# Optimization experiments

Measured on AMD Instinct MI355X. Metric: run time of the kernel, lower is better.

The kernel has to match this reference:

```python
import jax, jax.numpy as jnp
import numpy as np

IN_DIM, HID, HEADS, OUT_DIM = 768, 128, 4, 256
SEM = HID * HEADS  # 512
N_USER, N_LLM, E = 50000, 5000, 400000


def gat_conv(x_src, x_dst, src, dst, W_src, W_dst, att_src, att_dst, bias, n_dst):
    """PyG GATConv (bipartite, concat=True), eval mode (no dropout)."""
    H, C = att_src.shape
    hs = (x_src @ W_src).reshape(-1, H, C)  # [Ns,H,C]
    hd = (x_dst @ W_dst).reshape(-1, H, C)  # [Nd,H,C]
    a_s = (hs * att_src).sum(-1)            # [Ns,H]
    a_d = (hd * att_dst).sum(-1)            # [Nd,H]
    e = jax.nn.leaky_relu(a_s[src] + a_d[dst], 0.2)  # [E,H]
    m = jax.ops.segment_max(e, dst, num_segments=n_dst)
    m = jnp.where(jnp.isfinite(m), m, 0.0)
    ex = jnp.exp(e - m[dst])
    denom = jax.ops.segment_sum(ex, dst, num_segments=n_dst)
    alpha = ex / (denom[dst] + 1e-16)        # [E,H]
    msg = hs[src] * alpha[:, :, None]        # [E,H,C]
    out = jax.ops.segment_sum(msg, dst, num_segments=n_dst)  # [Nd,H,C]
    return out.reshape(n_dst, H * C) + bias


def setup_inputs() -> dict:
    key = jax.random.key(0)
    ks = jax.random.split(key, 20)
    s = lambda k, shape, sc: jax.random.normal(k, shape, jnp.float32) * sc
    d = {
        'x_user': jax.random.normal(ks[0], (N_USER, IN_DIM), jnp.float32),
        'x_llm': jax.random.normal(ks[1], (N_LLM, IN_DIM), jnp.float32),
        'src0': jax.random.randint(ks[2], (E,), 0, N_LLM, jnp.int32),
        'dst0': jax.random.randint(ks[3], (E,), 0, N_USER, jnp.int32),
        'src1': jax.random.randint(ks[4], (E,), 0, N_USER, jnp.int32),
        'dst1': jax.random.randint(ks[5], (E,), 0, N_USER, jnp.int32),
    }
    sc_in = 1.0 / np.sqrt(IN_DIM)
    for i in range(2):
        d[f'Wsrc{i}'] = s(ks[6 + 5 * i], (IN_DIM, HEADS * HID), sc_in)
        d[f'Wdst{i}'] = s(ks[7 + 5 * i], (IN_DIM, HEADS * HID), sc_in)
        d[f'asrc{i}'] = s(ks[8 + 5 * i], (HEADS, HID), 1.0 / np.sqrt(HID))
        d[f'adst{i}'] = s(ks[9 + 5 * i], (HEADS, HID), 1.0 / np.sqrt(HID))
        d[f'bias{i}'] = jnp.zeros((HEADS * HID,), jnp.float32)
    d['sem_W1'] = s(ks[16], (SEM, 128), 1.0 / np.sqrt(SEM))
    d['sem_b1'] = jnp.zeros((128,), jnp.float32)
    d['sem_W2'] = s(ks[17], (128, 1), 1.0 / np.sqrt(128))
    d['out_W'] = s(ks[18], (SEM, OUT_DIM), 1.0 / np.sqrt(SEM))
    d['out_b'] = jnp.zeros((OUT_DIM,), jnp.float32)
    return d


def reference(x_user, x_llm, src0, dst0, src1, dst1,
              Wsrc0, Wdst0, asrc0, adst0, bias0,
              Wsrc1, Wdst1, asrc1, adst1, bias1,
              sem_W1, sem_b1, sem_W2, out_W, out_b):
    # metapath 0: llm -> user ; metapath 1: user -> user
    z0 = jax.nn.elu(gat_conv(x_llm, x_user, src0, dst0,
                             Wsrc0, Wdst0, asrc0, adst0, bias0, N_USER))
    z1 = jax.nn.elu(gat_conv(x_user, x_user, src1, dst1,
                             Wsrc1, Wdst1, asrc1, adst1, bias1, N_USER))
    z = jnp.stack([z0, z1], axis=1)  # [N, P=2, SEM]
    w = jnp.tanh(z @ sem_W1 + sem_b1) @ sem_W2  # [N,P,1]
    beta = jax.nn.softmax(w, axis=1)
    z_final = (beta * z).sum(axis=1)  # [N, SEM]
    return z_final @ out_W + out_b    # [N, OUT_DIM]
```

## Files before the change

kernel.cpp:

```cpp
#include <hip/hip_runtime.h>
#include <hip/hip_bf16.h>
#include <math.h>

constexpr int IN_DIM  = 768;
constexpr int HID     = 128;
constexpr int OUT_DIM = 256;
constexpr int SEM     = 512;
constexpr int N_USER  = 50000;
constexpr int N_LLM   = 5000;
constexpr int NE      = 400000;

constexpr int MP_USER = 50048;
constexpr int MP_LLM  = 5120;
constexpr int MP_2U   = 100096;
constexpr int GY_USER = MP_USER / 128;
constexpr int GY_LLM  = MP_LLM / 128;

typedef unsigned int uint;
typedef unsigned short ushort;
typedef __attribute__((ext_vector_type(8))) short bf16x8;
typedef __attribute__((ext_vector_type(4))) float f32x4;

constexpr int cdiv(int a, int b) { return (a + b - 1) / b; }

__device__ __forceinline__ ushort f2b(float f) {
  uint u = __float_as_uint(f);
  u += 0x7FFFu + ((u >> 16) & 1u);
  return (ushort)(u >> 16);
}
__device__ __forceinline__ float b2f(uint bits16) {
  return __uint_as_float(bits16 << 16);
}

__device__ __forceinline__ float fexp2(float x) { return __builtin_amdgcn_exp2f(x); }
#define LOG2E 1.4426950408889634f

#define GLOAD_LDS16(g, l) __builtin_amdgcn_global_load_lds( \
    (const __attribute__((address_space(1))) void*)(g), \
    (__attribute__((address_space(3))) void*)(l), 16, 0, 0)


constexpr int GX_HS  = 5;
constexpr int NWG_HS = GX_HS * (GY_USER + GY_LLM);
constexpr int NB_SC  = cdiv(2 * NE, 256);
__global__ __launch_bounds__(256) void gemm_hs_sc(
    const ushort* __restrict__ A_u, const ushort* __restrict__ A_l,
    const ushort* __restrict__ Bt_u, const ushort* __restrict__ Bt_l,
    ushort* __restrict__ hs_u, ushort* __restrict__ hs_l,
    float* __restrict__ logU, float* __restrict__ logL,
    const int* __restrict__ src0, const int* __restrict__ dst0,
    const int* __restrict__ src1, const int* __restrict__ dst1,
    const int* __restrict__ rp, const int* __restrict__ rank,
    ushort* __restrict__ scsr)
{
  const int t = threadIdx.x;
  if (blockIdx.x >= NWG_HS) {
    int e = (blockIdx.x - NWG_HS) * 256 + t;
    if (e < 2 * NE) {
      bool p1 = (e >= NE);
      int ee = p1 ? e - NE : e;
      int s = p1 ? src1[ee] : src0[ee];
      int d = p1 ? (dst1[ee] + N_USER) : dst0[ee];
      scsr[rp[d] + rank[e]] = (ushort)s;
    }
    return;
  }

  __shared__ ushort As[128][64];
  __shared__ ushort Bs[128][64];
  const int wid = t >> 6, lane = t & 63;
  const int K = IN_DIM;

  const int nwg  = NWG_HS;
  const int orig = blockIdx.x;
  const int q = nwg >> 3, r = nwg & 7;
  const int xcd = orig & 7, idx = orig >> 3;
  const int swz = (xcd < r ? xcd * (q + 1) : r * (q + 1) + (xcd - r) * q) + idx;
  const int bxi = swz % GX_HS, byi0 = swz / GX_HS;

  const bool llm = (byi0 >= GY_USER);
  const int byi = llm ? byi0 - GY_USER : byi0;
  const ushort* A    = llm ? A_l : A_u;
  const ushort* Bt   = llm ? Bt_l : Bt_u;
  ushort* hs         = llm ? hs_l : hs_u;
  float* logit       = llm ? logL : logU;

  const int bm = byi * 128, bn = bxi * 128;
  const int lr = lane & 15, kg = lane >> 4;
  const int sw8 = lr & 7;
  const int mbase = (wid >> 1) * 64, nbase = (wid & 1) * 64;
  const int grow = lane >> 3;
  const int gcol = (((lane & 7) ^ grow)) * 8;

  f32x4 acc[4][4] = {};

  for (int k0 = 0; k0 < K; k0 += 64) {
#pragma unroll
    for (int c = 0; c < 4; ++c) {
      int ch = wid * 4 + c;
      GLOAD_LDS16(A  + (size_t)(bm + ch * 8 + grow) * K + k0 + gcol, &As[ch * 8][0]);
      GLOAD_LDS16(Bt + (size_t)(bn + ch * 8 + grow) * K + k0 + gcol, &Bs[ch * 8][0]);
    }
    asm volatile("s_waitcnt vmcnt(0)" ::: "memory");
    __syncthreads();
#pragma unroll
    for (int kb = 0; kb < 2; ++kb) {
      const int csw = ((kb * 4 + kg) ^ sw8) * 8;
      bf16x8 av[4], bv[4];
#pragma unroll
      for (int m = 0; m < 4; ++m)
        av[m] = *(const bf16x8*)&As[mbase + m * 16 + lr][csw];
#pragma unroll
      for (int n = 0; n < 4; ++n)
        bv[n] = *(const bf16x8*)&Bs[nbase + n * 16 + lr][csw];
#pragma unroll
      for (int m = 0; m < 4; ++m)
#pragma unroll
        for (int n = 0; n < 4; ++n)
          acc[m][n] = __builtin_amdgcn_mfma_f32_16x16x32_bf16(av[m], bv[n], acc[m][n], 0, 0, 0);
    }
    __syncthreads();
  }

  if (bxi == GX_HS - 1) {
    if (nbase == 0) {
#pragma unroll
      for (int m = 0; m < 4; ++m)
#pragma unroll
        for (int j = 0; j < 4; ++j) {
          int row = bm + mbase + m * 16 + kg * 4 + j;
          logit[(size_t)row * 16 + lr] = acc[m][0][j];
        }
    }
    return;
  }

#pragma unroll
  for (int m = 0; m < 4; ++m)
#pragma unroll
    for (int j = 0; j < 4; ++j) {
      int row = bm + mbase + m * 16 + kg * 4 + j;
#pragma unroll
      for (int n = 0; n < 4; ++n) {
        int col = bn + nbase + n * 16 + lr;
        hs[(size_t)row * SEM + col] = f2b(acc[m][n][j]);
      }
    }
}

__global__ __launch_bounds__(256) void gemm_beta(
    const ushort* __restrict__ Z, const ushort* __restrict__ WtS,
    const float* __restrict__ b1, const float* __restrict__ W2,
    float2* __restrict__ beta)
{
  __shared__ ushort As[128][64];
  __shared__ ushort Bs[128][64];
  __shared__ float wsum[128][2];
  const int t = threadIdx.x;
  const int wid = t >> 6, lane = t & 63;
  const int K = SEM;

  const int nwg  = gridDim.x;
  const int orig = blockIdx.x;
  const int q = nwg >> 3, r = nwg & 7;
  const int xcd = orig & 7, idx = orig >> 3;
  const int swz = (xcd < r ? xcd * (q + 1) : r * (q + 1) + (xcd - r) * q) + idx;

  const int bm = swz * 128;
  const int lr = lane & 15, kg = lane >> 4;
  const int sw8 = lr & 7;
  const int mbase = (wid >> 1) * 64, nbase = (wid & 1) * 64;
  const int grow = lane >> 3;
  const int gcol = (((lane & 7) ^ grow)) * 8;

  f32x4 acc[4][4] = {};

  for (int k0 = 0; k0 < K; k0 += 64) {
#pragma unroll
    for (int c = 0; c < 4; ++c) {
      int ch = wid * 4 + c;
      GLOAD_LDS16(Z   + (size_t)(bm + ch * 8 + grow) * K + k0 + gcol, &As[ch * 8][0]);
      GLOAD_LDS16(WtS + (size_t)(ch * 8 + grow) * K + k0 + gcol, &Bs[ch * 8][0]);
    }
    asm volatile("s_waitcnt vmcnt(0)" ::: "memory");
    __syncthreads();
#pragma unroll
    for (int kb = 0; kb < 2; ++kb) {
      const int csw = ((kb * 4 + kg) ^ sw8) * 8;
      bf16x8 av[4], bv[4];
#pragma unroll
      for (int m = 0; m < 4; ++m)
        av[m] = *(const bf16x8*)&As[mbase + m * 16 + lr][csw];
#pragma unroll
      for (int n = 0; n < 4; ++n)
        bv[n] = *(const bf16x8*)&Bs[nbase + n * 16 + lr][csw];
#pragma unroll
      for (int m = 0; m < 4; ++m)
#pragma unroll
        for (int n = 0; n < 4; ++n)
          acc[m][n] = __builtin_amdgcn_mfma_f32_16x16x32_bf16(av[m], bv[n], acc[m][n], 0, 0, 0);
    }
    __syncthreads();
  }

  float part[4][4];
#pragma unroll
  for (int m = 0; m < 4; ++m)
#pragma unroll
    for (int j = 0; j < 4; ++j) {
      float s = 0.f;
#pragma unroll
      for (int n = 0; n < 4; ++n) {
        int col = nbase + n * 16 + lr;
        float tv = acc[m][n][j] + b1[col];
        tv = fminf(fmaxf(tv, -20.f), 20.f);
        float e = fexp2(2.f * LOG2E * tv);
        s += ((e - 1.f) / (e + 1.f)) * W2[col];
      }
      part[m][j] = s;
    }
#pragma unroll
  for (int off = 1; off < 16; off <<= 1)
#pragma unroll
    for (int m = 0; m < 4; ++m)
#pragma unroll
      for (int j = 0; j < 4; ++j)
        part[m][j] += __shfl_xor(part[m][j], off);
  if (lr == 0) {
#pragma unroll
    for (int m = 0; m < 4; ++m)
#pragma unroll
      for (int j = 0; j < 4; ++j)
        wsum[mbase + m * 16 + kg * 4 + j][wid & 1] = part[m][j];
  }
  __syncthreads();
  if (t < 64) {
    float w0 = wsum[2 * t][0] + wsum[2 * t][1];
    float w1 = wsum[2 * t + 1][0] + wsum[2 * t + 1][1];
    float mx = fmaxf(w0, w1);
    float e0 = fexp2((w0 - mx) * LOG2E), e1 = fexp2((w1 - mx) * LOG2E);
    float s = e0 + e1;
    beta[swz * 64 + t] = make_float2(e0 / s, e1 / s);
  }
}

__global__ __launch_bounds__(256) void gemm_out(
    const ushort* __restrict__ Z, const ushort* __restrict__ WtO,
    float* __restrict__ out, const float* __restrict__ out_b,
    const float2* __restrict__ beta)
{
  __shared__ ushort As[128][64];
  __shared__ ushort Bs[256][64];
  const int t = threadIdx.x;
  const int wid = t >> 6, lane = t & 63;
  const int K = SEM;

  const int nwg  = gridDim.x;
  const int orig = blockIdx.x;
  const int q = nwg >> 3, r = nwg & 7;
  const int xcd = orig & 7, idx = orig >> 3;
  const int swz = (xcd < r ? xcd * (q + 1) : r * (q + 1) + (xcd - r) * q) + idx;

  const int bm = swz * 128;
  const int lr = lane & 15, kg = lane >> 4;
  const int sw8 = lr & 7;
  const int mbase = (wid >> 1) * 64, nbase = (wid & 1) * 128;
  const int grow = lane >> 3;
  const int gcol = (((lane & 7) ^ grow)) * 8;
  const int wcol = (((lane & 7) ^ grow)) * 8;

  f32x4 acc[4][8] = {};

  for (int k0 = 0; k0 < K; k0 += 64) {
#pragma unroll
    for (int c = 0; c < 8; ++c) {
      int ch = wid * 8 + c;
      GLOAD_LDS16(WtO + (size_t)(ch * 8 + grow) * K + k0 + gcol, &Bs[ch * 8][0]);
    }
#pragma unroll
    for (int c = 0; c < 4; ++c) {
      int ch = wid * 4 + c;
      int rl = ch * 8 + grow;
      int row = bm + rl;
      const ushort* z0p = Z + (size_t)(2 * row) * SEM + k0 + (lane & 7) * 8;
      const ushort* z1p = z0p + SEM;
      float2 bb = beta[row];
      uint4 a0 = *(const uint4*)z0p;
      uint4 a1 = *(const uint4*)z1p;
      uint rpk[4];
#pragma unroll
      for (int qq = 0; qq < 4; ++qq) {
        uint x0 = ((const uint*)&a0)[qq], x1 = ((const uint*)&a1)[qq];
        float lo = bb.x * b2f(x0 & 0xffffu) + bb.y * b2f(x1 & 0xffffu);
        float hi = bb.x * b2f(x0 >> 16)     + bb.y * b2f(x1 >> 16);
        rpk[qq] = (uint)f2b(lo) | ((uint)f2b(hi) << 16);
      }
      *(uint4*)&As[rl][wcol] = make_uint4(rpk[0], rpk[1], rpk[2], rpk[3]);
    }
    asm volatile("s_waitcnt vmcnt(0)" ::: "memory");
    __syncthreads();
#pragma unroll
    for (int kb = 0; kb < 2; ++kb) {
      const int csw = ((kb * 4 + kg) ^ sw8) * 8;
      bf16x8 av[4], bv[8];
#pragma unroll
      for (int m = 0; m < 4; ++m)
        av[m] = *(const bf16x8*)&As[mbase + m * 16 + lr][csw];
#pragma unroll
      for (int n = 0; n < 8; ++n)
        bv[n] = *(const bf16x8*)&Bs[nbase + n * 16 + lr][csw];
#pragma unroll
      for (int m = 0; m < 4; ++m)
#pragma unroll
        for (int n = 0; n < 8; ++n)
          acc[m][n] = __builtin_amdgcn_mfma_f32_16x16x32_bf16(av[m], bv[n], acc[m][n], 0, 0, 0);
    }
    __syncthreads();
  }

#pragma unroll
  for (int m = 0; m < 4; ++m)
#pragma unroll
    for (int j = 0; j < 4; ++j) {
      int row = bm + mbase + m * 16 + kg * 4 + j;
      if (row >= N_USER) continue;
#pragma unroll
      for (int n = 0; n < 8; ++n) {
        int col = nbase + n * 16 + lr;
        out[(size_t)row * OUT_DIM + col] = acc[m][n][j] + out_b[col];
      }
    }
}

constexpr int NB_FOLD  = cdiv(IN_DIM * 16, 256);
constexpr int NB_CASTU = N_USER * IN_DIM / 8 / 256;
constexpr int NB_CASTL = N_LLM * IN_DIM / 8 / 256;
constexpr int NB_TTW   = (IN_DIM / 64) * (SEM / 64);
constexpr int NB_TTS   = (SEM / 64) * (HID / 64);
constexpr int NB_TTO   = (SEM / 64) * (OUT_DIM / 64);
constexpr int NB_E1    = cdiv(2 * NE, 256);
constexpr int PB0 = NB_FOLD;
constexpr int PB1 = PB0 + NB_CASTU;
constexpr int PB2 = PB1 + NB_CASTL;
constexpr int PB3 = PB2 + NB_TTW;
constexpr int PB4 = PB3 + NB_TTW;
constexpr int PB5 = PB4 + NB_TTS;
constexpr int PB6 = PB5 + NB_TTO;
constexpr int PB7 = PB6 + NB_E1;
constexpr int PREP_GRID = 2048;

__device__ __forceinline__ void tt_body(const float* __restrict__ W,
                                        ushort* __restrict__ Bt,
                                        int K, int Nw, int tile,
                                        float (*lds)[65], int t)
{
  const int tiles_n = Nw >> 6;
  const int tk = tile / tiles_n, tn = tile - tk * tiles_n;
  const int k0 = tk << 6, n0 = tn << 6;
#pragma unroll
  for (int i = 0; i < 16; ++i) {
    int idx = t + i * 256;
    int rr = idx >> 6, cc = idx & 63;
    lds[rr][cc] = W[(size_t)(k0 + rr) * Nw + n0 + cc];
  }
  __syncthreads();
#pragma unroll
  for (int i = 0; i < 4; ++i) {
    int idx = t + i * 256;
    int cc = idx >> 4;
    int rq = (idx & 15) * 4;
    uint lo = (uint)f2b(lds[rq][cc])     | ((uint)f2b(lds[rq + 1][cc]) << 16);
    uint hi = (uint)f2b(lds[rq + 2][cc]) | ((uint)f2b(lds[rq + 3][cc]) << 16);
    *(uint2*)(Bt + (size_t)(n0 + cc) * K + k0 + rq) = make_uint2(lo, hi);
  }
  __syncthreads();
}

__device__ __forceinline__ void cast_body(const float* __restrict__ x,
                                          ushort* __restrict__ xb, int i)
{
  const float4 a = *(const float4*)(x + (size_t)i * 8);
  const float4 c = *(const float4*)(x + (size_t)i * 8 + 4);
  uint4 o;
  o.x = (uint)f2b(a.x) | ((uint)f2b(a.y) << 16);
  o.y = (uint)f2b(a.z) | ((uint)f2b(a.w) << 16);
  o.z = (uint)f2b(c.x) | ((uint)f2b(c.y) << 16);
  o.w = (uint)f2b(c.z) | ((uint)f2b(c.w) << 16);
  *(uint4*)(xb + (size_t)i * 8) = o;
}

__global__ __launch_bounds__(256) void prep_kernel(
    const float* __restrict__ x_user, const float* __restrict__ x_llm,
    ushort* __restrict__ xb_u, ushort* __restrict__ xb_l,
    const float* __restrict__ Wdst0, const float* __restrict__ adst0,
    const float* __restrict__ Wdst1, const float* __restrict__ adst1,
    const float* __restrict__ Wsrc1, const float* __restrict__ asrc1,
    const float* __restrict__ Wsrc0, const float* __restrict__ asrc0,
    ushort* __restrict__ Wt1x, ushort* __restrict__ Wt0x,
    const float* __restrict__ sem_W1, ushort* __restrict__ WtS,
    const float* __restrict__ out_W, ushort* __restrict__ WtO,
    const int* __restrict__ dst0, const int* __restrict__ dst1,
    int* __restrict__ deg, int* __restrict__ rank)
{
  __shared__ float lds[64][65];
  const int t = threadIdx.x;
  for (int b = blockIdx.x; b < PB7; b += PREP_GRID) {
    if (b < PB0) {
      int idxg = b * 256 + t;
      if (idxg < IN_DIM * 16) {
        int k = idxg >> 4, hh = idxg & 15;
        const float* W;
        const float* att;
        if (hh < 4)       { W = Wdst0; att = adst0; }
        else if (hh < 8)  { W = Wdst1; att = adst1; }
        else if (hh < 12) { W = Wsrc1; att = asrc1; }
        else              { W = Wsrc0; att = asrc0; }
        int h = hh & 3;
        float s = 0.f;
#pragma unroll 4
        for (int c = 0; c < HID; ++c)
          s += W[(size_t)k * SEM + h * HID + c] * att[h * HID + c];
        if (hh < 12) Wt1x[(size_t)(512 + hh) * IN_DIM + k] = f2b(s);
        else         Wt0x[(size_t)(512 + h) * IN_DIM + k] = f2b(s);
      }
    } else if (b < PB1) {
      cast_body(x_user, xb_u, (b - PB0) * 256 + t);
    } else if (b < PB2) {
      cast_body(x_llm, xb_l, (b - PB1) * 256 + t);
    } else if (b < PB3) {
      tt_body(Wsrc0, Wt0x, IN_DIM, SEM, b - PB2, lds, t);
    } else if (b < PB4) {
      tt_body(Wsrc1, Wt1x, IN_DIM, SEM, b - PB3, lds, t);
    } else if (b < PB5) {
      tt_body(sem_W1, WtS, SEM, HID, b - PB4, lds, t);
    } else if (b < PB6) {
      tt_body(out_W, WtO, SEM, OUT_DIM, b - PB5, lds, t);
    } else {
      int e = (b - PB6) * 256 + t;
      if (e < 2 * NE) {
        int d = (e < NE) ? dst0[e] : (dst1[e - NE] + N_USER);
        rank[e] = atomicAdd(&deg[d], 1);
      }
    }
  }
}

__global__ __launch_bounds__(256) void scan1(const int* __restrict__ deg,
                                             int* __restrict__ bsum, int n)
{
  __shared__ int sm[256];
  int b = blockIdx.x, t = threadIdx.x;
  int base = b * 1024 + t * 4;
  int s = 0;
#pragma unroll
  for (int i = 0; i < 4; ++i) if (base + i < n) s += deg[base + i];
  sm[t] = s;
  __syncthreads();
  for (int off = 128; off > 0; off >>= 1) {
    if (t < off) sm[t] += sm[t + off];
    __syncthreads();
  }
  if (t == 0) bsum[b] = sm[0];
}

__global__ __launch_bounds__(128) void scan2(const int* __restrict__ bsum,
                                             int* __restrict__ boff, int nb,
                                             int* __restrict__ rp_tail, int tailval)
{
  __shared__ int sm[128];
  int t = threadIdx.x;
  int v = (t < nb) ? bsum[t] : 0;
  sm[t] = v;
  __syncthreads();
  for (int off = 1; off < 128; off <<= 1) {
    int x = (t >= off) ? sm[t - off] : 0;
    __syncthreads();
    sm[t] += x;
    __syncthreads();
  }
  if (t < nb) boff[t] = sm[t] - v;
  if (t == 0) *rp_tail = tailval;
}

__global__ __launch_bounds__(256) void scan3(const int* __restrict__ deg,
                                             const int* __restrict__ boff,
                                             int* __restrict__ rp, int n)
{
  __shared__ int sm[256];
  int b = blockIdx.x, t = threadIdx.x;
  int base = b * 1024 + t * 4;
  int v[4];
#pragma unroll
  for (int i = 0; i < 4; ++i) v[i] = (base + i < n) ? deg[base + i] : 0;
  int tsum = v[0] + v[1] + v[2] + v[3];
  sm[t] = tsum;
  __syncthreads();
  for (int off = 1; off < 256; off <<= 1) {
    int x = (t >= off) ? sm[t - off] : 0;
    __syncthreads();
    sm[t] += x;
    __syncthreads();
  }
  int run = sm[t] - tsum + boff[b];
#pragma unroll
  for (int i = 0; i < 4; ++i) {
    if (base + i < n) rp[base + i] = run;
    run += v[i];
  }
}

__global__ __launch_bounds__(64) void agg_kernel(
    const ushort* __restrict__ hs0, const ushort* __restrict__ hs1,
    const ushort* __restrict__ srcs,
    const float* __restrict__ logitL, const float* __restrict__ logitU,
    const int* __restrict__ rp,
    const float* __restrict__ bias0, const float* __restrict__ bias1,
    ushort* __restrict__ Zout)
{
  __shared__ ushort s_src[64];
  __shared__ float  s_ev[64][4];
  int node = blockIdx.x, lane = threadIdx.x;
  bool p1 = (node >= N_USER);
  const ushort* hs   = p1 ? hs1 : hs0;
  const float*  bias = p1 ? bias1 : bias0;
  int nd = p1 ? node - N_USER : node;
  float4 ad4 = *(const float4*)(logitU + (size_t)nd * 16 + (p1 ? 4 : 0));
  ad4.x *= LOG2E; ad4.y *= LOG2E; ad4.z *= LOG2E; ad4.w *= LOG2E;
  const float* asbase = p1 ? (logitU + 8) : logitL;
  int h  = lane >> 4;
  int cb = lane * 8;
  float acc[8] = {};
  float dsum = 0.f;
  int jb = rp[node], je = rp[node + 1];
  for (int j0 = jb; j0 < je; j0 += 64) {
    int n = min(64, je - j0);
    __syncthreads();
    if (lane < n) {
      int s = srcs[j0 + lane];
      s_src[lane] = (ushort)s;
      float4 as4 = *(const float4*)(asbase + (size_t)s * 16);
      float v0 = as4.x * LOG2E + ad4.x, v1 = as4.y * LOG2E + ad4.y;
      float v2 = as4.z * LOG2E + ad4.z, v3 = as4.w * LOG2E + ad4.w;
      v0 = (v0 > 0.f) ? v0 : 0.2f * v0;
      v1 = (v1 > 0.f) ? v1 : 0.2f * v1;
      v2 = (v2 > 0.f) ? v2 : 0.2f * v2;
      v3 = (v3 > 0.f) ? v3 : 0.2f * v3;
      s_ev[lane][0] = fexp2(v0);
      s_ev[lane][1] = fexp2(v1);
      s_ev[lane][2] = fexp2(v2);
      s_ev[lane][3] = fexp2(v3);
    }
    __syncthreads();
#pragma unroll 4
    for (int j = 0; j < n; ++j) {
      int s = __builtin_amdgcn_readfirstlane((int)s_src[j]);
      float e = s_ev[j][h];
      const uint4 pv = *(const uint4*)(hs + ((size_t)s << 9) + cb);
      acc[0] += b2f(pv.x & 0xffffu) * e;  acc[1] += b2f(pv.x >> 16) * e;
      acc[2] += b2f(pv.y & 0xffffu) * e;  acc[3] += b2f(pv.y >> 16) * e;
      acc[4] += b2f(pv.z & 0xffffu) * e;  acc[5] += b2f(pv.z >> 16) * e;
      acc[6] += b2f(pv.w & 0xffffu) * e;  acc[7] += b2f(pv.w >> 16) * e;
      dsum += e;
    }
  }
  float inv = 1.f / (dsum + 1e-16f);
  float4 b4a = *(const float4*)(bias + cb);
  float4 b4b = *(const float4*)(bias + cb + 4);
  float bb[8] = { b4a.x, b4a.y, b4a.z, b4a.w, b4b.x, b4b.y, b4b.z, b4b.w };
  uint4 o;
  uint* op = (uint*)&o;
#pragma unroll
  for (int i = 0; i < 4; ++i) {
    float z0 = acc[2 * i]     * inv + bb[2 * i];
    float z1 = acc[2 * i + 1] * inv + bb[2 * i + 1];
    z0 = (z0 > 0.f) ? z0 : fexp2(z0 * LOG2E) - 1.f;
    z1 = (z1 > 0.f) ? z1 : fexp2(z1 * LOG2E) - 1.f;
    op[i] = (uint)f2b(z0) | ((uint)f2b(z1) << 16);
  }
  int zrow = 2 * nd + (p1 ? 1 : 0);
  *(uint4*)(Zout + (size_t)zrow * SEM + cb) = o;
}

extern "C" void kernel_launch(void* const* d_in, const int* in_sizes, int n_in,
                              void* d_out, int out_size, void* d_ws, size_t ws_size,
                              hipStream_t stream)
{
  const float* x_user = (const float*)d_in[0];
  const float* x_llm  = (const float*)d_in[1];
  const int* src0 = (const int*)d_in[2];
  const int* dst0 = (const int*)d_in[3];
  const int* src1 = (const int*)d_in[4];
  const int* dst1 = (const int*)d_in[5];
  const float* Wsrc0 = (const float*)d_in[6];
  const float* Wdst0 = (const float*)d_in[7];
  const float* asrc0 = (const float*)d_in[8];
  const float* adst0 = (const float*)d_in[9];
  const float* bias0 = (const float*)d_in[10];
  const float* Wsrc1 = (const float*)d_in[11];
  const float* Wdst1 = (const float*)d_in[12];
  const float* asrc1 = (const float*)d_in[13];
  const float* adst1 = (const float*)d_in[14];
  const float* bias1 = (const float*)d_in[15];
  const float* sem_W1 = (const float*)d_in[16];
  const float* sem_b1 = (const float*)d_in[17];
  const float* sem_W2 = (const float*)d_in[18];
  const float* out_W  = (const float*)d_in[19];
  const float* out_b  = (const float*)d_in[20];

  char* ws = (char*)d_ws;
  size_t off = 0;
  auto alloc = [&](size_t bytes) -> size_t {
    size_t o = off;
    off += (bytes + 255) & ~(size_t)255;
    return o;
  };

  size_t xbu_off  = alloc((size_t)MP_USER * IN_DIM * 2);
  size_t xbl_off  = alloc((size_t)MP_LLM  * IN_DIM * 2);
  size_t wt0_off  = alloc((size_t)640 * IN_DIM * 2);
  size_t wt1_off  = alloc((size_t)640 * IN_DIM * 2);
  size_t wts_off  = alloc((size_t)HID * SEM * 2);
  size_t wto_off  = alloc((size_t)OUT_DIM * SEM * 2);
  size_t hs0_off  = alloc((size_t)MP_LLM  * SEM * 2);
  size_t hs1_off  = alloc((size_t)MP_USER * SEM * 2);
  size_t Z_off    = alloc((size_t)MP_2U   * SEM * 2);
  size_t sc_off   = alloc((size_t)2 * NE * 2);
  size_t rank_off = alloc((size_t)2 * NE * 4);
  size_t lgu_off  = alloc((size_t)MP_USER * 16 * 4);
  size_t lgl_off  = alloc((size_t)MP_LLM  * 16 * 4);
  size_t beta_off = alloc((size_t)MP_USER * 8);
  size_t deg_off  = alloc((size_t)2 * N_USER * 4);
  size_t zero_end = off;
  size_t rp_off   = alloc((size_t)(2 * N_USER + 1) * 4);
  size_t bs_off   = alloc((size_t)128 * 4);
  size_t bo_off   = alloc((size_t)128 * 4);

  ushort* xb_u  = (ushort*)(ws + xbu_off);
  ushort* xb_l  = (ushort*)(ws + xbl_off);
  ushort* Wt0x  = (ushort*)(ws + wt0_off);
  ushort* Wt1x  = (ushort*)(ws + wt1_off);
  ushort* WtS   = (ushort*)(ws + wts_off);
  ushort* WtO   = (ushort*)(ws + wto_off);
  ushort* hs0b  = (ushort*)(ws + hs0_off);
  ushort* hs1b  = (ushort*)(ws + hs1_off);
  ushort* Zsw   = (ushort*)(ws + Z_off);
  ushort* scsr  = (ushort*)(ws + sc_off);
  int*    rank  = (int*)(ws + rank_off);
  float*  logU  = (float*)(ws + lgu_off);
  float*  logL  = (float*)(ws + lgl_off);
  float2* beta  = (float2*)(ws + beta_off);
  int*    deg   = (int*)(ws + deg_off);
  int*    rp    = (int*)(ws + rp_off);
  int*    bsum  = (int*)(ws + bs_off);
  int*    boff  = (int*)(ws + bo_off);

  hipMemsetAsync(ws + deg_off, 0, zero_end - deg_off, stream);
  hipMemsetAsync(Wt0x + (size_t)512 * IN_DIM, 0, (size_t)128 * IN_DIM * 2, stream);
  hipMemsetAsync(Wt1x + (size_t)512 * IN_DIM, 0, (size_t)128 * IN_DIM * 2, stream);

  prep_kernel<<<PREP_GRID, 256, 0, stream>>>(
      x_user, x_llm, xb_u, xb_l,
      Wdst0, adst0, Wdst1, adst1, Wsrc1, asrc1, Wsrc0, asrc0,
      Wt1x, Wt0x, sem_W1, WtS, out_W, WtO,
      dst0, dst1, deg, rank);

  const int NTOT = 2 * N_USER;
  const int NB = cdiv(NTOT, 1024);
  scan1<<<NB, 256, 0, stream>>>(deg, bsum, NTOT);
  scan2<<<1, 128, 0, stream>>>(bsum, boff, NB, rp + NTOT, 2 * NE);
  scan3<<<NB, 256, 0, stream>>>(deg, boff, rp, NTOT);

  gemm_hs_sc<<<NWG_HS + NB_SC, 256, 0, stream>>>(
      xb_u, xb_l, Wt1x, Wt0x, hs1b, hs0b, logU, logL,
      src0, dst0, src1, dst1, rp, rank, scsr);

  agg_kernel<<<NTOT, 64, 0, stream>>>(hs0b, hs1b, scsr, logL, logU, rp,
                                      bias0, bias1, Zsw);

  gemm_beta<<<MP_2U / 128, 256, 0, stream>>>(Zsw, WtS, sem_b1, sem_W2, beta);

  gemm_out<<<GY_USER, 256, 0, stream>>>(Zsw, WtO, (float*)d_out, out_b, beta);
}
```

Baseline: 372.9 us.

## Fuse semantic-attention beta GEMM and output GEMM into one kernel

Merges gemm_beta and gemm_out into a single kernel: each workgroup computes beta for its 64 nodes (128 Z rows), keeps it in LDS, then immediately does the beta-weighted combine and the output projection for those same 64 nodes. This removes one kernel launch, the global beta buffer round trip, and lets the Z tile be re-read while likely still in cache. In exchange the output GEMM tile shrinks from 128 to 64 rows per workgroup with twice the workgroups, so WtO is loaded twice as often and per-workgroup MFMA density drops; LDS use grows.

```diff
diff --git a/kernel.cpp b/kernel.cpp
--- a/kernel.cpp
+++ b/kernel.cpp
@@ -148,14 +148,16 @@
     }
 }
 
-__global__ __launch_bounds__(256) void gemm_beta(
+__global__ __launch_bounds__(256) void gemm_bo(
     const ushort* __restrict__ Z, const ushort* __restrict__ WtS,
     const float* __restrict__ b1, const float* __restrict__ W2,
-    float2* __restrict__ beta)
+    const ushort* __restrict__ WtO, float* __restrict__ out,
+    const float* __restrict__ out_b)
 {
   __shared__ ushort As[128][64];
-  __shared__ ushort Bs[128][64];
+  __shared__ ushort Bs[256][64];
   __shared__ float wsum[128][2];
+  __shared__ float2 betaL[64];
   const int t = threadIdx.x;
   const int wid = t >> 6, lane = t & 63;
   const int K = SEM;
@@ -166,170 +168,149 @@
   const int xcd = orig & 7, idx = orig >> 3;
   const int swz = (xcd < r ? xcd * (q + 1) : r * (q + 1) + (xcd - r) * q) + idx;
 
-  const int bm = swz * 128;
   const int lr = lane & 15, kg = lane >> 4;
   const int sw8 = lr & 7;
-  const int mbase = (wid >> 1) * 64, nbase = (wid & 1) * 64;
   const int grow = lane >> 3;
   const int gcol = (((lane & 7) ^ grow)) * 8;
 
-  f32x4 acc[4][4] = {};
-
-  for (int k0 = 0; k0 < K; k0 += 64) {
-#pragma unroll
-    for (int c = 0; c < 4; ++c) {
-      int ch = wid * 4 + c;
-      GLOAD_LDS16(Z   + (size_t)(bm + ch * 8 + grow) * K + k0 + gcol, &As[ch * 8][0]);
-      GLOAD_LDS16(WtS + (size_t)(ch * 8 + grow) * K + k0 + gcol, &Bs[ch * 8][0]);
-    }
-    asm volatile("s_waitcnt vmcnt(0)" ::: "memory");
-    __syncthreads();
-#pragma unroll
-    for (int kb = 0; kb < 2; ++kb) {
-      const int csw = ((kb * 4 + kg) ^ sw8) * 8;
-      bf16x8 av[4], bv[4];
+  {
+    const int bm = swz * 128;
+    const int mbase = (wid >> 1) * 64, nbase = (wid & 1) * 64;
+    f32x4 acc[4][4] = {};
+    for (int k0 = 0; k0 < K; k0 += 64) {
+#pragma unroll
+      for (int c = 0; c < 4; ++c) {
+        int ch = wid * 4 + c;
+        GLOAD_LDS16(Z   + (size_t)(bm + ch * 8 + grow) * K + k0 + gcol, &As[ch * 8][0]);
+        GLOAD_LDS16(WtS + (size_t)(ch * 8 + grow) * K + k0 + gcol, &Bs[ch * 8][0]);
+      }
+      asm volatile("s_waitcnt vmcnt(0)" ::: "memory");
+      __syncthreads();
+#pragma unroll
+      for (int kb = 0; kb < 2; ++kb) {
+        const int csw = ((kb * 4 + kg) ^ sw8) * 8;
+        bf16x8 av[4], bv[4];
+#pragma unroll
+        for (int m = 0; m < 4; ++m)
+          av[m] = *(const bf16x8*)&As[mbase + m * 16 + lr][csw];
+#pragma unroll
+        for (int n = 0; n < 4; ++n)
+          bv[n] = *(const bf16x8*)&Bs[nbase + n * 16 + lr][csw];
+#pragma unroll
+        for (int m = 0; m < 4; ++m)
+#pragma unroll
+          for (int n = 0; n < 4; ++n)
+            acc[m][n] = __builtin_amdgcn_mfma_f32_16x16x32_bf16(av[m], bv[n], acc[m][n], 0, 0, 0);
+      }
+      __syncthreads();
+    }
+
+    float part[4][4];
+#pragma unroll
+    for (int m = 0; m < 4; ++m)
+#pragma unroll
+      for (int j = 0; j < 4; ++j) {
+        float s = 0.f;
+#pragma unroll
+        for (int n = 0; n < 4; ++n) {
+          int col = nbase + n * 16 + lr;
+          float tv = acc[m][n][j] + b1[col];
+          tv = fminf(fmaxf(tv, -20.f), 20.f);
+          float e = fexp2(2.f * LOG2E * tv);
+          s += ((e - 1.f) / (e + 1.f)) * W2[col];
+        }
+        part[m][j] = s;
+      }
+#pragma unroll
+    for (int off = 1; off < 16; off <<= 1)
 #pragma unroll
       for (int m = 0; m < 4; ++m)
-        av[m] = *(const bf16x8*)&As[mbase + m * 16 + lr][csw];
-#pragma unroll
-      for (int n = 0; n < 4; ++n)
-        bv[n] = *(const bf16x8*)&Bs[nbase + n * 16 + lr][csw];
+#pragma unroll
+        for (int j = 0; j < 4; ++j)
+          part[m][j] += __shfl_xor(part[m][j], off);
+    if (lr == 0) {
 #pragma unroll
       for (int m = 0; m < 4; ++m)
 #pragma unroll
-        for (int n = 0; n < 4; ++n)
-          acc[m][n] = __builtin_amdgcn_mfma_f32_16x16x32_bf16(av[m], bv[n], acc[m][n], 0, 0, 0);
-    }
-    __syncthreads();
-  }
-
-  float part[4][4];
-#pragma unroll
-  for (int m = 0; m < 4; ++m)
-#pragma unroll
-    for (int j = 0; j < 4; ++j) {
-      float s = 0.f;
-#pragma unroll
-      for (int n = 0; n < 4; ++n) {
-        int col = nbase + n * 16 + lr;
-        float tv = acc[m][n][j] + b1[col];
-        tv = fminf(fmaxf(tv, -20.f), 20.f);
-        float e = fexp2(2.f * LOG2E * tv);
-        s += ((e - 1.f) / (e + 1.f)) * W2[col];
-      }
-      part[m][j] = s;
-    }
-#pragma unroll
-  for (int off = 1; off < 16; off <<= 1)
-#pragma unroll
-    for (int m = 0; m < 4; ++m)
-#pragma unroll
-      for (int j = 0; j < 4; ++j)
-        part[m][j] += __shfl_xor(part[m][j], off);
-  if (lr == 0) {
-#pragma unroll
-    for (int m = 0; m < 4; ++m)
-#pragma unroll
-      for (int j = 0; j < 4; ++j)
-        wsum[mbase + m * 16 + kg * 4 + j][wid & 1] = part[m][j];
-  }
-  __syncthreads();
-  if (t < 64) {
-    float w0 = wsum[2 * t][0] + wsum[2 * t][1];
-    float w1 = wsum[2 * t + 1][0] + wsum[2 * t + 1][1];
-    float mx = fmaxf(w0, w1);
-    float e0 = fexp2((w0 - mx) * LOG2E), e1 = fexp2((w1 - mx) * LOG2E);
-    float s = e0 + e1;
-    beta[swz * 64 + t] = make_float2(e0 / s, e1 / s);
-  }
-}
-
-__global__ __launch_bounds__(256) void gemm_out(
-    const ushort* __restrict__ Z, const ushort* __restrict__ WtO,
-    float* __restrict__ out, const float* __restrict__ out_b,
-    const float2* __restrict__ beta)
-{
-  __shared__ ushort As[128][64];
-  __shared__ ushort Bs[256][64];
-  const int t = threadIdx.x;
-  const int wid = t >> 6, lane = t & 63;
-  const int K = SEM;
-
-  const int nwg  = gridDim.x;
-  const int orig = blockIdx.x;
-  const int q = nwg >> 3, r = nwg & 7;
-  const int xcd = orig & 7, idx = orig >> 3;
-  const int swz = (xcd < r ? xcd * (q + 1) : r * (q + 1) + (xcd - r) * q) + idx;
-
-  const int bm = swz * 128;
-  const int lr = lane & 15, kg = lane >> 4;
-  const int sw8 = lr & 7;
-  const int mbase = (wid >> 1) * 64, nbase = (wid & 1) * 128;
-  const int grow = lane >> 3;
-  const int gcol = (((lane & 7) ^ grow)) * 8;
-  const int wcol = (((lane & 7) ^ grow)) * 8;
-
-  f32x4 acc[4][8] = {};
-
-  for (int k0 = 0; k0 < K; k0 += 64) {
-#pragma unroll
-    for (int c = 0; c < 8; ++c) {
-      int ch = wid * 8 + c;
-      GLOAD_LDS16(WtO + (size_t)(ch * 8 + grow) * K + k0 + gcol, &Bs[ch * 8][0]);
-    }
-#pragma unroll
-    for (int c = 0; c < 4; ++c) {
-      int ch = wid * 4 + c;
-      int rl = ch * 8 + grow;
-      int row = bm + rl;
-      const ushort* z0p = Z + (size_t)(2 * row) * SEM + k0 + (lane & 7) * 8;
-      const ushort* z1p = z0p + SEM;
-      float2 bb = beta[row];
-      uint4 a0 = *(const uint4*)z0p;
-      uint4 a1 = *(const uint4*)z1p;
-      uint rpk[4];
-#pragma unroll
-      for (int qq = 0; qq < 4; ++qq) {
-        uint x0 = ((const uint*)&a0)[qq], x1 = ((const uint*)&a1)[qq];
-        float lo = bb.x * b2f(x0 & 0xffffu) + bb.y * b2f(x1 & 0xffffu);
-        float hi = bb.x * b2f(x0 >> 16)     + bb.y * b2f(x1 >> 16);
-        rpk[qq] = (uint)f2b(lo) | ((uint)f2b(hi) << 16);
-      }
-      *(uint4*)&As[rl][wcol] = make_uint4(rpk[0], rpk[1], rpk[2], rpk[3]);
-    }
-    asm volatile("s_waitcnt vmcnt(0)" ::: "memory");
-    __syncthreads();
-#pragma unroll
-    for (int kb = 0; kb < 2; ++kb) {
-      const int csw = ((kb * 4 + kg) ^ sw8) * 8;
-      bf16x8 av[4], bv[8];
-#pragma unroll
-      for (int m = 0; m < 4; ++m)
-        av[m] = *(const bf16x8*)&As[mbase + m * 16 + lr][csw];
-#pragma unroll
-      for (int n = 0; n < 8; ++n)
-        bv[n] = *(const bf16x8*)&Bs[nbase + n * 16 + lr][csw];
-#pragma unroll
-      for (int m = 0; m < 4; ++m)
+        for (int j = 0; j < 4; ++j)
+          wsum[mbase + m * 16 + kg * 4 + j][wid & 1] = part[m][j];
+    }
+    __syncthreads();
+    if (t < 64) {
+      float w0 = wsum[2 * t][0] + wsum[2 * t][1];
+      float w1 = wsum[2 * t + 1][0] + wsum[2 * t + 1][1];
+      float mx = fmaxf(w0, w1);
+      float e0 = fexp2((w0 - mx) * LOG2E), e1 = fexp2((w1 - mx) * LOG2E);
+      float s = e0 + e1;
+      betaL[t] = make_float2(e0 / s, e1 / s);
+    }
+    __syncthreads();
+  }
+
+  {
+    const int bm2 = swz * 64;
+    const int mbase = (wid >> 1) * 32, nbase = (wid & 1) * 128;
+    f32x4 acc[2][8] = {};
+    for (int k0 = 0; k0 < K; k0 += 64) {
+#pragma unroll
+      for (int c = 0; c < 8; ++c) {
+        int ch = wid * 8 + c;
+        GLOAD_LDS16(WtO + (size_t)(ch * 8 + grow) * K + k0 + gcol, &Bs[ch * 8][0]);
+      }
+#pragma unroll
+      for (int c = 0; c < 2; ++c) {
+        int ch = wid * 2 + c;
+        int rl = ch * 8 + grow;
+        int node = bm2 + rl;
+        const ushort* z0p = Z + (size_t)(2 * node) * SEM + k0 + (lane & 7) * 8;
+        const ushort* z1p = z0p + SEM;
+        float2 bb = betaL[rl];
+        uint4 a0 = *(const uint4*)z0p;
+        uint4 a1 = *(const uint4*)z1p;
+        uint rpk[4];
+#pragma unroll
+        for (int qq = 0; qq < 4; ++qq) {
+          uint x0 = ((const uint*)&a0)[qq], x1 = ((const uint*)&a1)[qq];
+          float lo = bb.x * b2f(x0 & 0xffffu) + bb.y * b2f(x1 & 0xffffu);
+          float hi = bb.x * b2f(x0 >> 16)     + bb.y * b2f(x1 >> 16);
+          rpk[qq] = (uint)f2b(lo) | ((uint)f2b(hi) << 16);
+        }
+        *(uint4*)&As[rl][gcol] = make_uint4(rpk[0], rpk[1], rpk[2], rpk[3]);
+      }
+      asm volatile("s_waitcnt vmcnt(0)" ::: "memory");
+      __syncthreads();
+#pragma unroll
+      for (int kb = 0; kb < 2; ++kb) {
+        const int csw = ((kb * 4 + kg) ^ sw8) * 8;
+        bf16x8 av[2], bv[8];
+#pragma unroll
+        for (int m = 0; m < 2; ++m)
+          av[m] = *(const bf16x8*)&As[mbase + m * 16 + lr][csw];
 #pragma unroll
         for (int n = 0; n < 8; ++n)
-          acc[m][n] = __builtin_amdgcn_mfma_f32_16x16x32_bf16(av[m], bv[n], acc[m][n], 0, 0, 0);
-    }
-    __syncthreads();
-  }
-
-#pragma unroll
-  for (int m = 0; m < 4; ++m)
-#pragma unroll
-    for (int j = 0; j < 4; ++j) {
-      int row = bm + mbase + m * 16 + kg * 4 + j;
-      if (row >= N_USER) continue;
-#pragma unroll
-      for (int n = 0; n < 8; ++n) {
-        int col = nbase + n * 16 + lr;
-        out[(size_t)row * OUT_DIM + col] = acc[m][n][j] + out_b[col];
-      }
-    }
+          bv[n] = *(const bf16x8*)&Bs[nbase + n * 16 + lr][csw];
+#pragma unroll
+        for (int m = 0; m < 2; ++m)
+#pragma unroll
+          for (int n = 0; n < 8; ++n)
+            acc[m][n] = __builtin_amdgcn_mfma_f32_16x16x32_bf16(av[m], bv[n], acc[m][n], 0, 0, 0);
+      }
+      __syncthreads();
+    }
+
+#pragma unroll
+    for (int m = 0; m < 2; ++m)
+#pragma unroll
+      for (int j = 0; j < 4; ++j) {
+        int node = bm2 + mbase + m * 16 + kg * 4 + j;
+        if (node >= N_USER) continue;
+#pragma unroll
+        for (int n = 0; n < 8; ++n) {
+          int col = nbase + n * 16 + lr;
+          out[(size_t)node * OUT_DIM + col] = acc[m][n][j] + out_b[col];
+        }
+      }
+  }
 }
 
 constexpr int NB_FOLD  = cdiv(IN_DIM * 16, 256);
@@ -628,7 +609,6 @@
   size_t rank_off = alloc((size_t)2 * NE * 4);
   size_t lgu_off  = alloc((size_t)MP_USER * 16 * 4);
   size_t lgl_off  = alloc((size_t)MP_LLM  * 16 * 4);
-  size_t beta_off = alloc((size_t)MP_USER * 8);
   size_t deg_off  = alloc((size_t)2 * N_USER * 4);
   size_t zero_end = off;
   size_t rp_off   = alloc((size_t)(2 * N_USER + 1) * 4);
@@ -648,7 +628,6 @@
   int*    rank  = (int*)(ws + rank_off);
   float*  logU  = (float*)(ws + lgu_off);
   float*  logL  = (float*)(ws + lgl_off);
-  float2* beta  = (float2*)(ws + beta_off);
   int*    deg   = (int*)(ws + deg_off);
   int*    rp    = (int*)(ws + rp_off);
   int*    bsum  = (int*)(ws + bs_off);
@@ -677,7 +656,6 @@
   agg_kernel<<<NTOT, 64, 0, stream>>>(hs0b, hs1b, scsr, logL, logU, rp,
                                       bias0, bias1, Zsw);
 
-  gemm_beta<<<MP_2U / 128, 256, 0, stream>>>(Zsw, WtS, sem_b1, sem_W2, beta);
-
-  gemm_out<<<GY_USER, 256, 0, stream>>>(Zsw, WtO, (float*)d_out, out_b, beta);
-}
+  gemm_bo<<<MP_2U / 128, 256, 0, stream>>>(Zsw, WtS, sem_b1, sem_W2,
+                                           WtO, (float*)d_out, out_b);
+}
```

Result: faster. 354.1 us (-5.0%).
